# Kernel optimization log

Measured on AMD Instinct MI355X. Metric: run time of the kernel, lower is better.

The kernel has to match this reference:

```python
import jax, jax.numpy as jnp
import numpy as np

B, F, D = 4096, 39, 16          # batch, num_field, embedding_size
V = 1000000                     # num_feat (vocab)
H1, H2 = 128, 128               # cin_layer_sizes
INPUT_DIM = F * D               # 624
FC_DIM = H1 // 2 + H2           # 192 (split_half)
DEEP = [400, 400]
BN_EPS = 1e-5


def setup_inputs() -> dict:
    key = jax.random.key(0)
    ks = jax.random.split(key, 16)
    xav = lambda k, shp: jax.random.normal(k, shp, jnp.float32) * np.sqrt(2.0 / (shp[0] + shp[-1]))
    return {
        "feat_index": jax.random.randint(ks[0], (B, F), 0, V),
        "feat_value": jax.random.uniform(ks[1], (B, F), jnp.float32),
        "emb_table": xav(ks[2], (V, D)),
        "linear_w": xav(ks[3], (INPUT_DIM, 1)),
        "linear_b": jnp.zeros((1,), jnp.float32),
        "conv_w1": xav(ks[4], (H1, F, F)),          # (out, h_prev, m) == conv1d 1x1 weight reshaped
        "conv_b1": jnp.zeros((H1,), jnp.float32),
        "conv_w2": xav(ks[5], (H2, H1 // 2, F)),
        "conv_b2": jnp.zeros((H2,), jnp.float32),
        "deep_w1": xav(ks[6], (INPUT_DIM, DEEP[0])),
        "deep_b1": jnp.zeros((DEEP[0],), jnp.float32),
        "bn_g1": jnp.ones((DEEP[0],), jnp.float32),
        "bn_b1": jnp.zeros((DEEP[0],), jnp.float32),
        "deep_w2": xav(ks[7], (DEEP[0], DEEP[1])),
        "deep_b2": jnp.zeros((DEEP[1],), jnp.float32),
        "bn_g2": jnp.ones((DEEP[1],), jnp.float32),
        "bn_b2": jnpp if False else jnp.zeros((DEEP[1],), jnp.float32),
        "out_w": xav(ks[8], (1 + FC_DIM + DEEP[1], 1)),
        "out_b": jnp.zeros((1,), jnp.float32),
    }


def _bn(x, g, b):
    # torch BatchNorm1d in training mode: biased batch variance
    m = x.mean(axis=0)
    v = x.var(axis=0)
    return g * (x - m) * jax.lax.rsqrt(v + BN_EPS) + b


def reference(feat_index, feat_value, emb_table, linear_w, linear_b,
              conv_w1, conv_b1, conv_w2, conv_b2,
              deep_w1, deep_b1, bn_g1, bn_b1,
              deep_w2, deep_b2, bn_g2, bn_b2,
              out_w, out_b):
    e = emb_table[feat_index]                      # [B, F, D]
    flat = e.reshape(e.shape[0], -1)               # [B, F*D]
    linear_part = flat @ linear_w + linear_b       # [B, 1]

    # CIN: fused outer-product + 1x1 conv (x_k[b,o,d] = sum_{h,m} W[o,h,m] x_prev[b,h,d] x0[b,m,d])
    x0 = e
    h1 = jax.nn.relu(jnp.einsum('bhd,bmd,ohm->bod', x0, x0, conv_w1) + conv_b1[None, :, None])
    nxt, hi1 = jnp.split(h1, 2, axis=1)            # split_half
    h2 = jax.nn.relu(jnp.einsum('bhd,bmd,ohm->bod', nxt, x0, conv_w2) + conv_b2[None, :, None])
    res = jnp.concatenate([hi1, h2], axis=1).sum(axis=2)   # [B, FC_DIM]

    # Deep tower (dropout off / deterministic)
    y = jax.nn.relu(_bn(flat @ deep_w1 + deep_b1, bn_g1, bn_b1))
    y = jax.nn.relu(_bn(y @ deep_w2 + deep_b2, bn_g2, bn_b2))

    cat = jnp.concatenate([linear_part, res, y], axis=1)   # [B, 593]
    return cat @ out_w + out_b
```

## Files before the change

### kernel.cpp

```cpp
#include <hip/hip_runtime.h>

#define BATCH   4096
#define NF      39
#define ED      16
#define IN_DIM  624
#define DW      400
#define BN_EPS  1e-5f
#define NK16    156
#define AK1     640
#define NKS1    20
#define NKS2    13
#define WCOL    416

typedef __attribute__((ext_vector_type(8))) short short8;
typedef __attribute__((ext_vector_type(16))) float f32x16;
typedef __attribute__((ext_vector_type(4))) float f32x4;
typedef __attribute__((ext_vector_type(2))) float f32x2;
typedef unsigned short u16;

__device__ inline unsigned pack_hi2(float a, float b) {
  return __builtin_amdgcn_perm(__float_as_uint(b), __float_as_uint(a), 0x07060302u);
}
__device__ inline unsigned bf16_rne(float f) {
  unsigned u = __float_as_uint(f);
  u += 0x7fff + ((u >> 16) & 1);
  return u >> 16;
}
__device__ inline float bf2f(u16 v) { return __uint_as_float((unsigned)v << 16); }

#define CIN_E (NK16 * 128 * 16)
#define D1_E  (NKS1 * WCOL * 32)
#define D2_E  (NKS2 * WCOL * 32)
#define PREP_E (CIN_E + D1_E + D2_E + 1600)
#define PREP_B ((PREP_E + 255) / 256)
#define GATH_B (BATCH / 4)

__global__ __launch_bounds__(256) void k_gp(const int* __restrict__ idx,
    const float* __restrict__ emb, const float* __restrict__ lw,
    const float* __restrict__ lb, const float* __restrict__ w1,
    const float* __restrict__ w2, const float* __restrict__ dw1,
    const float* __restrict__ dw2, u16* __restrict__ flatb,
    float* __restrict__ lp, u16* __restrict__ wp1, u16* __restrict__ wp2,
    u16* __restrict__ wpd1, u16* __restrict__ wpd2, float* __restrict__ gstat) {
  int t = threadIdx.x;
  if (blockIdx.x < GATH_B) {
    int lane = t & 63;
    int b = blockIdx.x * 4 + (t >> 6);
    int sj = (lane < NF) ? idx[b * NF + lane] : 0;
    float acc = 0.f;
#pragma unroll
    for (int i = 0; i < 10; i++) {
      int e = lane + i * 64;
      if (e < IN_DIM) {
        int f = e >> 4;
        int row = __shfl(sj, f);
        float v = emb[(size_t)row * ED + (e & 15)];
        flatb[(size_t)b * AK1 + e] = (u16)bf16_rne(v);
        acc = fmaf(v, lw[e], acc);
      } else {
        flatb[(size_t)b * AK1 + e] = 0;
      }
    }
#pragma unroll
    for (int k = 1; k < 64; k <<= 1) acc += __shfl_xor(acc, k);
    if (lane == 0) lp[b] = acc + lb[0];
  } else {
    int e = (blockIdx.x - GATH_B) * 256 + t;
    if (e < CIN_E) {
      int k16 = e >> 11, r = e & 2047, col = r >> 4, kk = r & 15;
      int k = k16 * 16 + kk, h = k & 63, m = k >> 6;
      float v1 = (h < NF) ? w1[(size_t)col * (NF * NF) + h * NF + m] : 0.f;
      float v2 = w2[(size_t)col * (64 * NF) + h * NF + m];
      wp1[e] = (u16)bf16_rne(v1);
      wp2[e] = (u16)bf16_rne(v2);
    } else if (e < CIN_E + D1_E) {
      int e2 = e - CIN_E;
      int ksg = e2 / (WCOL * 32), r = e2 - ksg * (WCOL * 32);
      int col = r >> 5, kk = r & 31;
      int k = ksg * 32 + kk;
      wpd1[e2] = (k < IN_DIM && col < DW) ? (u16)bf16_rne(dw1[(size_t)k * DW + col]) : 0;
    } else if (e < CIN_E + D1_E + D2_E) {
      int e2 = e - CIN_E - D1_E;
      int ksg = e2 / (WCOL * 32), r = e2 - ksg * (WCOL * 32);
      int col = r >> 5, kk = r & 31;
      int k = ksg * 32 + kk;
      wpd2[e2] = (k < DW && col < DW) ? (u16)bf16_rne(dw2[(size_t)k * DW + col]) : 0;
    } else if (e < PREP_E) {
      gstat[e - CIN_E - D1_E - D2_E] = 0.f;
    }
  }
}

template <bool LAY2>
__global__ __launch_bounds__(256, 4) void k_cin32(
    const u16* __restrict__ flatb, const u16* __restrict__ nxtg,
    const u16* __restrict__ wp, const float* __restrict__ bias,
    u16* __restrict__ nxt_out, float* __restrict__ res) {
  __shared__ u16 bsm[2][1024];
  int t = threadIdx.x;
  int w = t >> 6, lane = t & 63;
  int col = lane & 31, khalf = lane >> 5;
  int si = (lane >> 4) & 1, d = lane & 15;
  int bid = blockIdx.x;
  int b0 = (bid >> 1) * 8 + w * 2;
  int c0 = (bid & 1) * 64;
  int b = b0 + si;
  const u16* fb = flatb + (size_t)b * AK1;

  const u16* gchunk = wp + (size_t)(c0 + ((t >> 6) & 1) * 32 + (t & 31)) * 16
                         + ((t >> 5) & 1) * 8;

  f32x2 sp[4][4];
  if (LAY2) {
#pragma unroll
    for (int s = 0; s < 4; s++) {
      uint4 v = *(const uint4*)(nxtg + (((size_t)b * 16 + d) * 64 + s * 16 + khalf * 8));
      unsigned uu[4] = {v.x, v.y, v.z, v.w};
#pragma unroll
      for (int w4 = 0; w4 < 4; w4++)
        sp[s][w4] = (f32x2){__uint_as_float(uu[w4] << 16),
                            __uint_as_float(uu[w4] & 0xffff0000u)};
    }
  } else {
#pragma unroll
    for (int s = 0; s < 4; s++)
#pragma unroll
      for (int w4 = 0; w4 < 4; w4++) {
        int h0 = s * 16 + khalf * 8 + 2 * w4;
        int h1 = h0 + 1;
        float f0 = (h0 < NF) ? bf2f(fb[h0 * 16 + d]) : 0.f;
        float f1 = (h1 < NF) ? bf2f(fb[h1 * 16 + d]) : 0.f;
        sp[s][w4] = (f32x2){f0, f1};
      }
  }

  f32x16 acc[2];
#pragma unroll
  for (int nt = 0; nt < 2; nt++)
#pragma unroll
    for (int r = 0; r < 16; r++) acc[nt][r] = 0.f;

  uint4 stg;
  if (t < 128) {
    stg = *(const uint4*)gchunk;
    *(uint4*)&bsm[0][(size_t)t * 8] = stg;
  }
  __syncthreads();
  if (t < 128) stg = *(const uint4*)(gchunk + 2048);

  float xv = bf2f(fb[d]);
  float xvn;
  int rdoff0 = khalf * 256 + col * 8;
  int rdoff1 = 512 + khalf * 256 + col * 8;

  for (int mg = 0; mg < 13; mg++) {
#pragma unroll
    for (int j = 0; j < 12; j++) {
      int k16 = mg * 12 + j;
      int cur = k16 & 1;
      if (j == 0 || j == 4 || j == 8) {
        int mn = mg * 3 + (j >> 2) + 1;
        xvn = bf2f(fb[mn * 16 + d]);
      }
      short8 bfr0 = *(const short8*)&bsm[cur][rdoff0];
      short8 bfr1 = *(const short8*)&bsm[cur][rdoff1];
      int s = j & 3;
      union { unsigned u[4]; short8 v; } a;
      f32x2 xv2 = (f32x2){xv, xv};
#pragma unroll
      for (int w4 = 0; w4 < 4; w4++) {
        f32x2 p = sp[s][w4] * xv2;
        a.u[w4] = pack_hi2(p[0], p[1]);
      }
      acc[0] = __builtin_amdgcn_mfma_f32_32x32x16_bf16(a.v, bfr0, acc[0], 0, 0, 0);
      acc[1] = __builtin_amdgcn_mfma_f32_32x32x16_bf16(a.v, bfr1, acc[1], 0, 0, 0);
      if (k16 + 1 < NK16 && t < 128) {
        *(uint4*)&bsm[cur ^ 1][(size_t)t * 8] = stg;
        if (k16 + 2 < NK16)
          stg = *(const uint4*)(gchunk + (size_t)(k16 + 2) * 2048);
      }
      if (s == 3) xv = xvn;
      __syncthreads();
    }
  }

#pragma unroll
  for (int nt = 0; nt < 2; nt++) {
    int o = c0 + nt * 32 + col;
    float bi = bias[o];
    if (!LAY2 && c0 == 0) {
#pragma unroll
      for (int r = 0; r < 16; r++) {
        int si2 = r >> 3;
        int dd = (r & 3) + 8 * ((r >> 2) & 1) + 4 * khalf;
        float v = fmaxf(acc[nt][r] + bi, 0.f);
        nxt_out[((size_t)(b0 + si2) * 16 + dd) * 64 + o] = (u16)bf16_rne(v);
      }
    } else {
      float p0 = 0.f, p1 = 0.f;
#pragma unroll
      for (int r = 0; r < 8; r++)  p0 += fmaxf(acc[nt][r] + bi, 0.f);
#pragma unroll
      for (int r = 8; r < 16; r++) p1 += fmaxf(acc[nt][r] + bi, 0.f);
      p0 += __shfl_xor(p0, 32);
      p1 += __shfl_xor(p1, 32);
      if (khalf == 0) {
        int ri = LAY2 ? (64 + o) : (o - 64);
        res[(size_t)b0 * 192 + ri] = p0;
        res[(size_t)(b0 + 1) * 192 + ri] = p1;
      }
    }
  }
}

template <bool BN_A, int NKS, int KREAL, int AK>
__global__ __launch_bounds__(256) void k_gemm_mfma(
    const u16* __restrict__ Abf, const float* __restrict__ Af32,
    const u16* __restrict__ wp, const float* __restrict__ bias,
    const float* __restrict__ gsIn, const float* __restrict__ gs2In,
    const float* __restrict__ bng, const float* __restrict__ bnb,
    float* __restrict__ C, float* __restrict__ gs, float* __restrict__ gs2) {
  __shared__ float lsS[NKS * 32], lsH[NKS * 32];
  __shared__ float lred[64];
  int t = threadIdx.x;
  if (BN_A) {
    for (int c = t; c < NKS * 32; c += 256) {
      float sc = 0.f, sh = 0.f;
      if (c < DW) {
        float m = gsIn[c] * (1.f / BATCH);
        float var = gs2In[c] * (1.f / BATCH) - m * m;
        sc = bng[c] * rsqrtf(var + BN_EPS);
        sh = bnb[c] - m * sc;
      }
      lsS[c] = sc; lsH[c] = sh;
    }
  }
  if (t < 64) lred[t] = 0.f;
  __syncthreads();

  int w = t >> 6, lane = t & 63;
  int nl = lane & 15, q = lane >> 4;
  int row = blockIdx.x * 64 + w * 16 + nl;
  int c0 = blockIdx.y * 32;
  f32x4 acc[2];
  acc[0] = (f32x4){0.f, 0.f, 0.f, 0.f};
  acc[1] = (f32x4){0.f, 0.f, 0.f, 0.f};

  short8 araw[2]; f32x4 fraw0[2], fraw1[2]; short8 braw[2][2];
  auto loadA_raw = [&](int ksg, int buf) {
    int kb = ksg * 32 + q * 8;
    if (!BN_A) {
      araw[buf] = *(const short8*)(Abf + (size_t)row * AK + kb);
    } else {
      if (kb + 8 <= KREAL) {
        fraw0[buf] = *(const f32x4*)(Af32 + (size_t)row * KREAL + kb);
        fraw1[buf] = *(const f32x4*)(Af32 + (size_t)row * KREAL + kb + 4);
      } else {
        fraw0[buf] = (f32x4){0.f,0.f,0.f,0.f};
        fraw1[buf] = (f32x4){0.f,0.f,0.f,0.f};
      }
    }
    const u16* wb = wp + (size_t)ksg * (WCOL * 32) + (size_t)(c0 + nl) * 32 + q * 8;
    braw[buf][0] = *(const short8*)wb;
    braw[buf][1] = *(const short8*)(wb + 16 * 32);
  };
  auto cookA = [&](int ksg, int buf) -> short8 {
    if (!BN_A) return araw[buf];
    int kb = ksg * 32 + q * 8;
    f32x4 s0 = *(const f32x4*)&lsS[kb], h0 = *(const f32x4*)&lsH[kb];
    f32x4 s1 = *(const f32x4*)&lsS[kb + 4], h1 = *(const f32x4*)&lsH[kb + 4];
    union { unsigned u[4]; short8 s; } a;
    float v0 = fmaxf(fmaf(fraw0[buf][0], s0[0], h0[0]), 0.f);
    float v1 = fmaxf(fmaf(fraw0[buf][1], s0[1], h0[1]), 0.f);
    float v2 = fmaxf(fmaf(fraw0[buf][2], s0[2], h0[2]), 0.f);
    float v3 = fmaxf(fmaf(fraw0[buf][3], s0[3], h0[3]), 0.f);
    float v4 = fmaxf(fmaf(fraw1[buf][0], s1[0], h1[0]), 0.f);
    float v5 = fmaxf(fmaf(fraw1[buf][1], s1[1], h1[1]), 0.f);
    float v6 = fmaxf(fmaf(fraw1[buf][2], s1[2], h1[2]), 0.f);
    float v7 = fmaxf(fmaf(fraw1[buf][3], s1[3], h1[3]), 0.f);
    a.u[0] = bf16_rne(v0) | (bf16_rne(v1) << 16);
    a.u[1] = bf16_rne(v2) | (bf16_rne(v3) << 16);
    a.u[2] = bf16_rne(v4) | (bf16_rne(v5) << 16);
    a.u[3] = bf16_rne(v6) | (bf16_rne(v7) << 16);
    return a.s;
  };

  loadA_raw(0, 0);
#pragma unroll 4
  for (int ksg = 0; ksg < NKS; ksg++) {
    int cur = ksg & 1;
    if (ksg + 1 < NKS) loadA_raw(ksg + 1, cur ^ 1);
    short8 afr = cookA(ksg, cur);
    acc[0] = __builtin_amdgcn_mfma_f32_16x16x32_bf16(afr, braw[cur][0], acc[0], 0, 0, 0);
    acc[1] = __builtin_amdgcn_mfma_f32_16x16x32_bf16(afr, braw[cur][1], acc[1], 0, 0, 0);
  }

  int rbase = blockIdx.x * 64 + w * 16 + q * 4;
#pragma unroll
  for (int nt = 0; nt < 2; nt++) {
    int col = c0 + nt * 16 + nl;
    if (col < DW) {
      float bi = bias[col];
      float s = 0.f, s2 = 0.f;
#pragma unroll
      for (int r = 0; r < 4; r++) {
        float v = acc[nt][r] + bi;
        C[(size_t)(rbase + r) * DW + col] = v;
        s += v; s2 = fmaf(v, v, s2);
      }
      s += __shfl_xor(s, 16); s2 += __shfl_xor(s2, 16);
      s += __shfl_xor(s, 32); s2 += __shfl_xor(s2, 32);
      if (q == 0) {
        atomicAdd(&lred[nt * 16 + nl], s);
        atomicAdd(&lred[32 + nt * 16 + nl], s2);
      }
    }
  }
  __syncthreads();
  if (t < 32) {
    int col = c0 + t;
    if (col < DW) atomicAdd(&gs[col], lred[t]);
  } else if (t < 64) {
    int col = c0 + t - 32;
    if (col < DW) atomicAdd(&gs2[col], lred[t]);
  }
}

__global__ __launch_bounds__(256) void k_final(const float* __restrict__ lp,
    const float* __restrict__ res, const float* __restrict__ y2,
    const float* __restrict__ gB, const float* __restrict__ gB2,
    const float* __restrict__ g2, const float* __restrict__ bb2,
    const float* __restrict__ ow, const float* __restrict__ ob,
    float* __restrict__ out) {
  __shared__ float lsS[DW], lsH[DW];
  int t = threadIdx.x;
  for (int c = t; c < DW; c += 256) {
    float m = gB[c] * (1.f / BATCH);
    float var = gB2[c] * (1.f / BATCH) - m * m;
    float sc = g2[c] * rsqrtf(var + BN_EPS);
    lsS[c] = sc;
    lsH[c] = bb2[c] - m * sc;
  }
  __syncthreads();
  int lane = t & 63, w = t >> 6;
  int b = blockIdx.x * 4 + w;
  float acc = 0.f;
  for (int j = lane; j < 593; j += 64) {
    float v;
    if (j == 0)       v = lp[b];
    else if (j < 193) v = res[(size_t)b * 192 + (j - 1)];
    else {
      int c = j - 193;
      v = fmaxf(fmaf(y2[(size_t)b * DW + c], lsS[c], lsH[c]), 0.f);
    }
    acc = fmaf(v, ow[j], acc);
  }
#pragma unroll
  for (int k = 1; k < 64; k <<= 1) acc += __shfl_xor(acc, k);
  if (lane == 0) out[b] = acc + ob[0];
}

extern "C" void kernel_launch(void* const* d_in, const int* in_sizes, int n_in,
                              void* d_out, int out_size, void* d_ws, size_t ws_size,
                              hipStream_t stream) {
  const int*   feat_index = (const int*)d_in[0];
  const float* emb = (const float*)d_in[2];
  const float* lw  = (const float*)d_in[3];
  const float* lb  = (const float*)d_in[4];
  const float* w1  = (const float*)d_in[5];
  const float* b1  = (const float*)d_in[6];
  const float* w2  = (const float*)d_in[7];
  const float* b2  = (const float*)d_in[8];
  const float* dw1 = (const float*)d_in[9];
  const float* db1 = (const float*)d_in[10];
  const float* g1  = (const float*)d_in[11];
  const float* bb1 = (const float*)d_in[12];
  const float* dw2 = (const float*)d_in[13];
  const float* db2 = (const float*)d_in[14];
  const float* g2  = (const float*)d_in[15];
  const float* bb2 = (const float*)d_in[16];
  const float* ow  = (const float*)d_in[17];
  const float* ob  = (const float*)d_in[18];

  float* ws   = (float*)d_ws;
  u16*  flatb = (u16*)ws;
  float* y1   = ws + 1310720;
  float* res  = ws + 2949120;
  float* lp   = ws + 3735552;
  float* gA   = ws + 3741248;
  float* gA2  = gA + 400;
  float* gB   = gA2 + 400;
  float* gB2  = gB + 400;
  u16*  nxtg  = (u16*)(ws + 3742848);
  float* y2   = ws + 3742848;
  u16*  wp1   = (u16*)(ws + 5840000);
  u16*  wp2   = (u16*)(ws + 5999744);
  u16*  wpd1  = (u16*)(ws + 6159488);
  u16*  wpd2  = (u16*)(ws + 6292608);
  float* out  = (float*)d_out;

  k_gp<<<GATH_B + PREP_B, 256, 0, stream>>>(feat_index, emb, lw, lb, w1, w2,
      dw1, dw2, flatb, lp, wp1, wp2, wpd1, wpd2, gA);
  k_cin32<false><<<1024, 256, 0, stream>>>(flatb, nullptr, wp1, b1, nxtg, res);
  k_cin32<true><<<1024, 256, 0, stream>>>(flatb, nxtg, wp2, b2, nullptr, res);
  k_gemm_mfma<false, NKS1, IN_DIM, AK1><<<dim3(BATCH / 64, 13), 256, 0, stream>>>(
      flatb, nullptr, wpd1, db1, nullptr, nullptr, nullptr, nullptr, y1, gA, gA2);
  k_gemm_mfma<true, NKS2, DW, 0><<<dim3(BATCH / 64, 13), 256, 0, stream>>>(
      nullptr, y1, wpd2, db2, gA, gA2, g1, bb1, y2, gB, gB2);
  k_final<<<BATCH / 4, 256, 0, stream>>>(lp, res, y2, gB, gB2, g2, bb2, ow, ob, out);
}
```

Before: 273.3 us.

## Co-schedule CIN layers with deep-tower GEMMs in fused launches, double k-step staging

Merges each CIN layer with the matching deep-tower GEMM into one launch, interleaving GEMM blocks among CIN blocks by block index. The two independent workloads can then share the GPU at the same time instead of running back to back in four launches. The CIN loop now stages two k16 slices per barrier, with all 256 threads loading, which halves the number of __syncthreads. To avoid an aliasing conflict, y2 moves to a separate workspace region when the workspace is large enough. The cost is larger shared memory per block and the GEMM running at the CIN kernel's launch bounds, which may limit its occupancy.

```diff
diff --git a/kernel.cpp b/kernel.cpp
--- a/kernel.cpp
+++ b/kernel.cpp
@@ -92,23 +92,22 @@
 }
 
 template <bool LAY2>
-__global__ __launch_bounds__(256, 4) void k_cin32(
+__device__ __forceinline__ void cin_body(int cidx, int t, u16 (*bsm)[4096],
     const u16* __restrict__ flatb, const u16* __restrict__ nxtg,
     const u16* __restrict__ wp, const float* __restrict__ bias,
     u16* __restrict__ nxt_out, float* __restrict__ res) {
-  __shared__ u16 bsm[2][1024];
-  int t = threadIdx.x;
   int w = t >> 6, lane = t & 63;
   int col = lane & 31, khalf = lane >> 5;
   int si = (lane >> 4) & 1, d = lane & 15;
-  int bid = blockIdx.x;
-  int b0 = (bid >> 1) * 8 + w * 2;
-  int c0 = (bid & 1) * 64;
+  int b0 = (cidx >> 1) * 8 + w * 2;
+  int c0 = (cidx & 1) * 64;
   int b = b0 + si;
   const u16* fb = flatb + (size_t)b * AK1;
 
-  const u16* gchunk = wp + (size_t)(c0 + ((t >> 6) & 1) * 32 + (t & 31)) * 16
-                         + ((t >> 5) & 1) * 8;
+  int c = t & 127, tp = t >> 7;
+  const u16* gch = wp + (size_t)(c0 + ((c >> 6) & 1) * 32 + (c & 31)) * 16
+                      + ((c >> 5) & 1) * 8;
+  int stoff = tp * 1024 + c * 8;
 
   f32x2 sp[4][4];
   if (LAY2) {
@@ -140,48 +139,42 @@
 #pragma unroll
     for (int r = 0; r < 16; r++) acc[nt][r] = 0.f;
 
-  uint4 stg;
-  if (t < 128) {
-    stg = *(const uint4*)gchunk;
-    *(uint4*)&bsm[0][(size_t)t * 8] = stg;
-  }
+  uint4 stg = *(const uint4*)(gch + (size_t)tp * 2048);
+  *(uint4*)&bsm[0][stoff] = stg;
   __syncthreads();
-  if (t < 128) stg = *(const uint4*)(gchunk + 2048);
+  stg = *(const uint4*)(gch + (size_t)(2 + tp) * 2048);
 
   float xv = bf2f(fb[d]);
-  float xvn;
+  float xvn = 0.f;
   int rdoff0 = khalf * 256 + col * 8;
   int rdoff1 = 512 + khalf * 256 + col * 8;
 
-  for (int mg = 0; mg < 13; mg++) {
-#pragma unroll
-    for (int j = 0; j < 12; j++) {
-      int k16 = mg * 12 + j;
-      int cur = k16 & 1;
-      if (j == 0 || j == 4 || j == 8) {
-        int mn = mg * 3 + (j >> 2) + 1;
-        xvn = bf2f(fb[mn * 16 + d]);
-      }
-      short8 bfr0 = *(const short8*)&bsm[cur][rdoff0];
-      short8 bfr1 = *(const short8*)&bsm[cur][rdoff1];
-      int s = j & 3;
+  for (int p = 0; p < 78; p++) {
+    int cur = p & 1;
+#pragma unroll
+    for (int j = 0; j < 2; j++) {
+      int k16 = 2 * p + j;
+      int s = k16 & 3;
+      if (s == 0) xvn = bf2f(fb[((k16 >> 2) + 1) * 16 + d]);
+      short8 bfr0 = *(const short8*)&bsm[cur][j * 1024 + rdoff0];
+      short8 bfr1 = *(const short8*)&bsm[cur][j * 1024 + rdoff1];
       union { unsigned u[4]; short8 v; } a;
       f32x2 xv2 = (f32x2){xv, xv};
 #pragma unroll
       for (int w4 = 0; w4 < 4; w4++) {
-        f32x2 p = sp[s][w4] * xv2;
-        a.u[w4] = pack_hi2(p[0], p[1]);
+        f32x2 pr = sp[s][w4] * xv2;
+        a.u[w4] = pack_hi2(pr[0], pr[1]);
       }
       acc[0] = __builtin_amdgcn_mfma_f32_32x32x16_bf16(a.v, bfr0, acc[0], 0, 0, 0);
       acc[1] = __builtin_amdgcn_mfma_f32_32x32x16_bf16(a.v, bfr1, acc[1], 0, 0, 0);
-      if (k16 + 1 < NK16 && t < 128) {
-        *(uint4*)&bsm[cur ^ 1][(size_t)t * 8] = stg;
-        if (k16 + 2 < NK16)
-          stg = *(const uint4*)(gchunk + (size_t)(k16 + 2) * 2048);
-      }
       if (s == 3) xv = xvn;
-      __syncthreads();
-    }
+    }
+    if (p + 1 < 78) {
+      *(uint4*)&bsm[cur ^ 1][stoff] = stg;
+      if (p + 2 < 78)
+        stg = *(const uint4*)(gch + (size_t)(2 * (p + 2) + tp) * 2048);
+    }
+    __syncthreads();
   }
 
 #pragma unroll
@@ -214,15 +207,13 @@
 }
 
 template <bool BN_A, int NKS, int KREAL, int AK>
-__global__ __launch_bounds__(256) void k_gemm_mfma(
+__device__ __forceinline__ void gemm_body(int gx, int gy, int t,
+    float* lsS, float* lsH, float* lred,
     const u16* __restrict__ Abf, const float* __restrict__ Af32,
     const u16* __restrict__ wp, const float* __restrict__ bias,
     const float* __restrict__ gsIn, const float* __restrict__ gs2In,
     const float* __restrict__ bng, const float* __restrict__ bnb,
     float* __restrict__ C, float* __restrict__ gs, float* __restrict__ gs2) {
-  __shared__ float lsS[NKS * 32], lsH[NKS * 32];
-  __shared__ float lred[64];
-  int t = threadIdx.x;
   if (BN_A) {
     for (int c = t; c < NKS * 32; c += 256) {
       float sc = 0.f, sh = 0.f;
@@ -240,8 +231,8 @@
 
   int w = t >> 6, lane = t & 63;
   int nl = lane & 15, q = lane >> 4;
-  int row = blockIdx.x * 64 + w * 16 + nl;
-  int c0 = blockIdx.y * 32;
+  int row = gx * 64 + w * 16 + nl;
+  int c0 = gy * 32;
   f32x4 acc[2];
   acc[0] = (f32x4){0.f, 0.f, 0.f, 0.f};
   acc[1] = (f32x4){0.f, 0.f, 0.f, 0.f};
@@ -295,7 +286,7 @@
     acc[1] = __builtin_amdgcn_mfma_f32_16x16x32_bf16(afr, braw[cur][1], acc[1], 0, 0, 0);
   }
 
-  int rbase = blockIdx.x * 64 + w * 16 + q * 4;
+  int rbase = gx * 64 + w * 16 + q * 4;
 #pragma unroll
   for (int nt = 0; nt < 2; nt++) {
     int col = c0 + nt * 16 + nl;
@@ -324,6 +315,64 @@
     int col = c0 + t - 32;
     if (col < DW) atomicAdd(&gs2[col], lred[t]);
   }
+}
+
+template <bool PH2>
+__device__ __forceinline__ void gemm_go(int gx, int gy, int t,
+    float* lsS, float* lsH, float* lred,
+    const u16* Abf, const float* Af32, const u16* wpd, const float* dbias,
+    const float* gsIn, const float* gs2In, const float* bng, const float* bnb,
+    float* C, float* gs, float* gs2) {
+  if (PH2)
+    gemm_body<true, NKS2, DW, 0>(gx, gy, t, lsS, lsH, lred, Abf, Af32, wpd,
+        dbias, gsIn, gs2In, bng, bnb, C, gs, gs2);
+  else
+    gemm_body<false, NKS1, IN_DIM, AK1>(gx, gy, t, lsS, lsH, lred, Abf, Af32,
+        wpd, dbias, gsIn, gs2In, bng, bnb, C, gs, gs2);
+}
+
+template <bool PH2>
+__global__ __launch_bounds__(256, 4) void k_fused(
+    const u16* __restrict__ flatb, const u16* __restrict__ nxtg,
+    const u16* __restrict__ wpc, const float* __restrict__ cbias,
+    u16* __restrict__ nxt_out, float* __restrict__ res,
+    const u16* __restrict__ Abf, const float* __restrict__ Af32,
+    const u16* __restrict__ wpd, const float* __restrict__ dbias,
+    const float* __restrict__ gsIn, const float* __restrict__ gs2In,
+    const float* __restrict__ bng, const float* __restrict__ bnb,
+    float* __restrict__ C, float* __restrict__ gs, float* __restrict__ gs2) {
+  __shared__ u16 bsm[2][4096];
+  __shared__ float lsS[640], lsH[640], lred[64];
+  int bid = blockIdx.x, t = threadIdx.x;
+  if (bid < 1664 && (bid & 1)) {
+    gemm_go<PH2>((bid >> 1) & 63, (bid >> 1) >> 6, t, lsS, lsH, lred,
+                 Abf, Af32, wpd, dbias, gsIn, gs2In, bng, bnb, C, gs, gs2);
+  } else {
+    int cidx = (bid < 1664) ? (bid >> 1) : (bid - 832);
+    cin_body<PH2>(cidx, t, bsm, flatb, nxtg, wpc, cbias, nxt_out, res);
+  }
+}
+
+template <bool LAY2>
+__global__ __launch_bounds__(256, 4) void k_cin32(
+    const u16* __restrict__ flatb, const u16* __restrict__ nxtg,
+    const u16* __restrict__ wp, const float* __restrict__ bias,
+    u16* __restrict__ nxt_out, float* __restrict__ res) {
+  __shared__ u16 bsm[2][4096];
+  cin_body<LAY2>(blockIdx.x, threadIdx.x, bsm, flatb, nxtg, wp, bias,
+                 nxt_out, res);
+}
+
+template <bool PH2>
+__global__ __launch_bounds__(256) void k_gemm_mfma(
+    const u16* __restrict__ Abf, const float* __restrict__ Af32,
+    const u16* __restrict__ wp, const float* __restrict__ bias,
+    const float* __restrict__ gsIn, const float* __restrict__ gs2In,
+    const float* __restrict__ bng, const float* __restrict__ bnb,
+    float* __restrict__ C, float* __restrict__ gs, float* __restrict__ gs2) {
+  __shared__ float lsS[640], lsH[640], lred[64];
+  gemm_go<PH2>(blockIdx.x, blockIdx.y, threadIdx.x, lsS, lsH, lred,
+               Abf, Af32, wp, bias, gsIn, gs2In, bng, bnb, C, gs, gs2);
 }
 
 __global__ __launch_bounds__(256) void k_final(const float* __restrict__ lp,
@@ -392,20 +441,35 @@
   float* gB   = gA2 + 400;
   float* gB2  = gB + 400;
   u16*  nxtg  = (u16*)(ws + 3742848);
-  float* y2   = ws + 3742848;
   u16*  wp1   = (u16*)(ws + 5840000);
   u16*  wp2   = (u16*)(ws + 5999744);
   u16*  wpd1  = (u16*)(ws + 6159488);
   u16*  wpd2  = (u16*)(ws + 6292608);
   float* out  = (float*)d_out;
 
+  bool bigws = ws_size >= (size_t)8017536 * 4;
+  float* y2  = bigws ? (ws + 6379136) : (ws + 3742848);
+
   k_gp<<<GATH_B + PREP_B, 256, 0, stream>>>(feat_index, emb, lw, lb, w1, w2,
       dw1, dw2, flatb, lp, wp1, wp2, wpd1, wpd2, gA);
-  k_cin32<false><<<1024, 256, 0, stream>>>(flatb, nullptr, wp1, b1, nxtg, res);
-  k_cin32<true><<<1024, 256, 0, stream>>>(flatb, nxtg, wp2, b2, nullptr, res);
-  k_gemm_mfma<false, NKS1, IN_DIM, AK1><<<dim3(BATCH / 64, 13), 256, 0, stream>>>(
-      flatb, nullptr, wpd1, db1, nullptr, nullptr, nullptr, nullptr, y1, gA, gA2);
-  k_gemm_mfma<true, NKS2, DW, 0><<<dim3(BATCH / 64, 13), 256, 0, stream>>>(
-      nullptr, y1, wpd2, db2, gA, gA2, g1, bb1, y2, gB, gB2);
-  k_final<<<BATCH / 4, 256, 0, stream>>>(lp, res, y2, gB, gB2, g2, bb2, ow, ob, out);
-}
+  if (bigws) {
+    k_fused<false><<<1856, 256, 0, stream>>>(
+        flatb, nullptr, wp1, b1, nxtg, res,
+        flatb, nullptr, wpd1, db1, nullptr, nullptr, nullptr, nullptr,
+        y1, gA, gA2);
+    k_fused<true><<<1856, 256, 0, stream>>>(
+        flatb, nxtg, wp2, b2, nullptr, res,
+        nullptr, y1, wpd2, db2, gA, gA2, g1, bb1,
+        y2, gB, gB2);
+  } else {
+    k_cin32<false><<<1024, 256, 0, stream>>>(flatb, nullptr, wp1, b1, nxtg, res);
+    k_cin32<true><<<1024, 256, 0, stream>>>(flatb, nxtg, wp2, b2, nullptr, res);
+    k_gemm_mfma<false><<<dim3(BATCH / 64, 13), 256, 0, stream>>>(
+        flatb, nullptr, wpd1, db1, nullptr, nullptr, nullptr, nullptr,
+        y1, gA, gA2);
+    k_gemm_mfma<true><<<dim3(BATCH / 64, 13), 256, 0, stream>>>(
+        nullptr, y1, wpd2, db2, gA, gA2, g1, bb1, y2, gB, gB2);
+  }
+  k_final<<<BATCH / 4, 256, 0, stream>>>(lp, res, y2, gB, gB2, g2, bb2,
+                                         ow, ob, out);
+}
```

After: 310.4 us. +13.6%, slower.
